# Kernel tuning notes

Measured on AMD Instinct MI355X. Metric: run time of the kernel, lower is better.

Reference implementation:

```python
import jax, jax.numpy as jnp
import numpy as np

CLIP_TEMPERATURE = 1.0


def setup_inputs() -> dict:
    key = jax.random.key(0)
    k1, k2 = jax.random.split(key)
    N, D = 16384, 256
    x = jax.random.normal(k1, (N, D), dtype=jnp.float32)
    y = jax.random.normal(k2, (N, D), dtype=jnp.float32)
    return {"x": x, "y": y}


def reference(x, y):
    # logits[i, j] = <x_i, y_j> / T ; labels are the diagonal (i-th text matches i-th image)
    logits = jnp.einsum('id,jd->ij', x, y) / CLIP_TEMPERATURE  # [N, N]
    N = logits.shape[0]
    diag_idx = jnp.arange(N)
    # CrossEntropy(logits, labels=arange) == -mean(diag(log_softmax(logits, axis=1)))
    lsm_row = jax.nn.log_softmax(logits, axis=1)  # image -> text
    lsm_col = jax.nn.log_softmax(logits, axis=0)  # text  -> image (== log_softmax(logits.T, axis=1).T)
    loss_row = -jnp.mean(lsm_row[diag_idx, diag_idx])
    loss_col = -jnp.mean(lsm_col[diag_idx, diag_idx])
    return (loss_row + loss_col) * 0.5
```

## Files before the change

kernel.cpp:

```cpp
#include <hip/hip_runtime.h>
#include <hip/hip_bf16.h>

#define NN 16384
#define DD 256
#define PANEL 128
#define JCOLS 128
#define BK 32
#define NT 8
#define NJ 16
#define THREADS 256
#define A_BYTES (PANEL * DD * 2)
#define B_BYTES (JCOLS * BK * 2)
#define SHIFT_C 64.0f
#define LOG2E 1.4426950408889634f

typedef __attribute__((ext_vector_type(4))) float f32x4;
typedef __attribute__((ext_vector_type(8))) short bf16x8;

#if __has_builtin(__builtin_amdgcn_exp2f)
#define EXP2F(x) __builtin_amdgcn_exp2f(x)
#else
#define EXP2F(x) exp2f(x)
#endif

__device__ __forceinline__ unsigned pkbf(float a, float b) {
  float2 t; t.x = a; t.y = b;
  __hip_bfloat162 h = __float22bfloat162_rn(t);
  union { __hip_bfloat162 h; unsigned u; } cv;
  cv.h = h;
  return cv.u;
}

__device__ __forceinline__ float rowsum16_dpp(float v) {
  union { float f; int i; } x, t;
  x.f = v;
  t.i = __builtin_amdgcn_update_dpp(0, x.i, 0x111, 0xf, 0xf, true); x.f += t.f;
  t.i = __builtin_amdgcn_update_dpp(0, x.i, 0x112, 0xf, 0xf, true); x.f += t.f;
  t.i = __builtin_amdgcn_update_dpp(0, x.i, 0x114, 0xf, 0xf, true); x.f += t.f;
  t.i = __builtin_amdgcn_update_dpp(0, x.i, 0x118, 0xf, 0xf, true); x.f += t.f;
  return x.f;
}

__global__ __launch_bounds__(256) void cvt_kernel(
    const float* __restrict__ X, const float* __restrict__ Y,
    unsigned short* __restrict__ Xb, unsigned short* __restrict__ Yb) {
  const int groups_per_arr = NN * DD / 8;
  int g = blockIdx.x * 256 + threadIdx.x;
  const float* src;
  unsigned short* dst;
  if (g < groups_per_arr) { src = X; dst = Xb; }
  else { src = Y; dst = Yb; g -= groups_per_arr; }
  float4 a = ((const float4*)src)[(size_t)g * 2];
  float4 b = ((const float4*)src)[(size_t)g * 2 + 1];
  uint4 p = { pkbf(a.x, a.y), pkbf(a.z, a.w), pkbf(b.x, b.y), pkbf(b.z, b.w) };
  ((uint4*)dst)[g] = p;
}

__global__ __launch_bounds__(THREADS, 2) void clip_gemm(
    const unsigned short* __restrict__ Xb, const unsigned short* __restrict__ Yb,
    float* __restrict__ rowsum, float* __restrict__ colsum,
    float* __restrict__ diagsum) {
  __shared__ __align__(16) unsigned char sm[A_BYTES + 2 * B_BYTES];

  const int tid = threadIdx.x;
  const int bid = blockIdx.x;
  const int colgroup = bid & 7;
  const int panel = bid >> 3;
  const int rowbase = panel * PANEL;
  const int colbase = colgroup * (NJ * JCOLS);

  const unsigned short* xb = Xb + (size_t)rowbase * DD;
  const unsigned short* ybg = Yb + (size_t)colbase * DD;

  const int wid = tid >> 6, lane = tid & 63;
  const int wm = wid >> 1, wn = wid & 1;
  const int lm = lane & 15, lk = lane >> 4;

#pragma unroll
  for (int p = 0; p < 16; ++p) {
    const int s = p * 256 + tid;
    const int row = s >> 5;
    const int g = (s & 31) ^ (row & 7);
    __builtin_amdgcn_global_load_lds(
        (const __attribute__((address_space(1))) unsigned*)(xb + row * DD + g * 8),
        (__attribute__((address_space(3))) unsigned*)(sm + s * 16), 16, 0, 0);
  }

  int bsrc[2], bdst[2];
#pragma unroll
  for (int p = 0; p < 2; ++p) {
    const int s = p * 256 + tid;
    const int col = s >> 2;
    const int g = (s & 3) ^ (col & 3);
    bsrc[p] = col * DD + g * 8;
    bdst[p] = A_BYTES + s * 16;
  }

#define GLOADB(jn, tn, buf)                                                    \
  {                                                                            \
    _Pragma("unroll")                                                          \
    for (int p = 0; p < 2; ++p)                                                \
      __builtin_amdgcn_global_load_lds(                                        \
          (const __attribute__((address_space(1))) unsigned*)(ybg + (size_t)(jn) * (JCOLS * DD) + bsrc[p] + (tn) * BK), \
          (__attribute__((address_space(3))) unsigned*)(sm + (buf) * B_BYTES + bdst[p]), \
          16, 0, 0);                                                           \
  }

#define RDA(m, t)                                                              \
  (*(const bf16x8*)(sm + (wm * 64 + (m) * 16 + lm) * (DD * 2) +                \
                    ((((t) * 4 + lk) ^ (lm & 7)) << 4)))
#define RDB(nf, buf)                                                           \
  (*(const bf16x8*)(sm + A_BYTES + (buf) * B_BYTES +                           \
                    (wn * 64 + (nf) * 16 + lm) * (BK * 2) +                    \
                    ((lk ^ (lm & 3)) << 4)))

  f32x4 acc[4][4] = {};
  float rowacc[4][4];
#pragma unroll
  for (int m = 0; m < 4; ++m)
#pragma unroll
    for (int r = 0; r < 4; ++r) rowacc[m][r] = 0.f;
  float dsum = 0.f;
  const float negC = -(SHIFT_C * LOG2E);

  GLOADB(0, 0, 0);

  for (int j = 0; j < NJ; ++j) {
#pragma unroll
    for (int t = 0; t < NT; ++t) {
      __syncthreads();
      if (t < NT - 1) { GLOADB(j, t + 1, (t + 1) & 1); }
      else if (j < NJ - 1) { GLOADB(j + 1, 0, 0); }
      const int buf = t & 1;
      bf16x8 b0[4];
#pragma unroll
      for (int nf = 0; nf < 4; ++nf) b0[nf] = RDB(nf, buf);
#pragma unroll
      for (int m = 0; m < 4; ++m) {
        const bf16x8 a0 = RDA(m, t);
#pragma unroll
        for (int nf = 0; nf < 4; ++nf)
          acc[m][nf] = __builtin_amdgcn_mfma_f32_16x16x32_bf16(a0, b0[nf], acc[m][nf], 0, 0, 0);
      }
    }

    const int jc0 = colbase + j * JCOLS;
    float colacc[4] = {0.f, 0.f, 0.f, 0.f};
#pragma unroll
    for (int m = 0; m < 4; ++m)
#pragma unroll
      for (int nf = 0; nf < 4; ++nf)
#pragma unroll
        for (int r = 0; r < 4; ++r) {
          float e = EXP2F(__builtin_fmaf(acc[m][nf][r], LOG2E, negC));
          rowacc[m][r] += e;
          colacc[nf] += e;
        }
    if (jc0 == rowbase) {
#pragma unroll
      for (int m = 0; m < 4; ++m)
#pragma unroll
        for (int nf = 0; nf < 4; ++nf)
#pragma unroll
          for (int r = 0; r < 4; ++r) {
            const int rr = wm * 64 + m * 16 + lk * 4 + r;
            const int cc = wn * 64 + nf * 16 + lm;
            if (rr == cc) dsum += acc[m][nf][r];
          }
    }
#pragma unroll
    for (int nf = 0; nf < 4; ++nf) {
      float v = colacc[nf];
      v += __shfl_xor(v, 16);
      v += __shfl_xor(v, 32);
      if (lk == 0)
        atomicAdd(&colsum[jc0 + wn * 64 + nf * 16 + lm], v);
    }
    const f32x4 z4 = {0.f, 0.f, 0.f, 0.f};
#pragma unroll
    for (int m = 0; m < 4; ++m)
#pragma unroll
      for (int nf = 0; nf < 4; ++nf) acc[m][nf] = z4;
  }
#undef GLOADB
#undef RDA
#undef RDB

  {
    float d = dsum;
    d += __shfl_xor(d, 1);
    d += __shfl_xor(d, 2);
    d += __shfl_xor(d, 4);
    d += __shfl_xor(d, 8);
    d += __shfl_xor(d, 16);
    d += __shfl_xor(d, 32);
    if (lane == 0 && d != 0.f) atomicAdd(diagsum, d);
  }
#pragma unroll
  for (int m = 0; m < 4; ++m)
#pragma unroll
    for (int r = 0; r < 4; ++r) {
      float v = rowsum16_dpp(rowacc[m][r]);
      if (lm == 15)
        atomicAdd(&rowsum[rowbase + wm * 64 + m * 16 + lk * 4 + r], v);
    }
}

__global__ __launch_bounds__(256) void clip_main_fb(
    const float* __restrict__ X, const float* __restrict__ Y,
    float* __restrict__ rowsum, float* __restrict__ colsum,
    float* __restrict__ diagsum) {
  __shared__ __align__(16) unsigned char smem[2 * 128 * 64 * 2];
  unsigned char* smA = smem;
  unsigned char* smB = smem + 128 * 64 * 2;

  const int tid = threadIdx.x;
  const int bid = blockIdx.x;
  const int swz = (bid & 7) * 2048 + (bid >> 3);
  const int brow = swz >> 7;
  const int bcol = swz & 127;

  const float* xb = X + (size_t)brow * 128 * DD;
  const float* yb = Y + (size_t)bcol * 128 * DD;

  const int wid = tid >> 6, lane = tid & 63;
  const int wm = wid >> 1, wn = wid & 1;
  const int lm = lane & 15, lk = lane >> 4;

  f32x4 acc[4][4] = {};

  for (int ks = 0; ks < 4; ++ks) {
    const int kbase = ks * 64;
    if (ks) __syncthreads();
#pragma unroll
    for (int i = 0; i < 4; ++i) {
      const int c = tid + i * 256;
      const int row = c >> 3, slot = c & 7;
      const int boff = row * 128 + ((slot << 4) ^ ((row & 7) << 4));
      const float* ga = xb + row * DD + kbase + (slot << 3);
      float4 a0 = *(const float4*)ga;
      float4 a1 = *(const float4*)(ga + 4);
      uint4 pa = { pkbf(a0.x, a0.y), pkbf(a0.z, a0.w),
                   pkbf(a1.x, a1.y), pkbf(a1.z, a1.w) };
      *(uint4*)(smA + boff) = pa;
      const float* gb = yb + row * DD + kbase + (slot << 3);
      float4 b0 = *(const float4*)gb;
      float4 b1 = *(const float4*)(gb + 4);
      uint4 pb = { pkbf(b0.x, b0.y), pkbf(b0.z, b0.w),
                   pkbf(b1.x, b1.y), pkbf(b1.z, b1.w) };
      *(uint4*)(smB + boff) = pb;
    }
    __syncthreads();

#pragma unroll
    for (int kk = 0; kk < 2; ++kk) {
      const int kboff = kk * 64 + lk * 16;
      bf16x8 a[4], b[4];
#pragma unroll
      for (int m = 0; m < 4; ++m) {
        const int row = wm * 64 + m * 16 + lm;
        a[m] = *(const bf16x8*)(smA + row * 128 + (kboff ^ ((row & 7) << 4)));
      }
#pragma unroll
      for (int n = 0; n < 4; ++n) {
        const int row = wn * 64 + n * 16 + lm;
        b[n] = *(const bf16x8*)(smB + row * 128 + (kboff ^ ((row & 7) << 4)));
      }
#pragma unroll
      for (int m = 0; m < 4; ++m)
#pragma unroll
        for (int n = 0; n < 4; ++n)
          acc[m][n] = __builtin_amdgcn_mfma_f32_16x16x32_bf16(a[m], b[n], acc[m][n], 0, 0, 0);
    }
  }

  float rowacc[4][4];
  float colacc[4];
#pragma unroll
  for (int m = 0; m < 4; ++m)
#pragma unroll
    for (int r = 0; r < 4; ++r) rowacc[m][r] = 0.f;
#pragma unroll
  for (int n = 0; n < 4; ++n) colacc[n] = 0.f;

  const float negC = -(SHIFT_C * LOG2E);
#pragma unroll
  for (int m = 0; m < 4; ++m)
#pragma unroll
    for (int n = 0; n < 4; ++n)
#pragma unroll
      for (int r = 0; r < 4; ++r) {
        float e = EXP2F(__builtin_fmaf(acc[m][n][r], LOG2E, negC));
        rowacc[m][r] += e;
        colacc[n] += e;
      }

  if (brow == bcol && wm == wn) {
    float dsum = 0.f;
#pragma unroll
    for (int m = 0; m < 4; ++m)
#pragma unroll
      for (int n = 0; n < 4; ++n)
#pragma unroll
        for (int r = 0; r < 4; ++r) {
          const int rr = m * 16 + lk * 4 + r;
          const int cc = n * 16 + lm;
          if (rr == cc) dsum += acc[m][n][r];
        }
    dsum += __shfl_xor(dsum, 1);
    dsum += __shfl_xor(dsum, 2);
    dsum += __shfl_xor(dsum, 4);
    dsum += __shfl_xor(dsum, 8);
    dsum += __shfl_xor(dsum, 16);
    dsum += __shfl_xor(dsum, 32);
    if (lane == 0) atomicAdd(diagsum, dsum);
  }

#pragma unroll
  for (int m = 0; m < 4; ++m)
#pragma unroll
    for (int r = 0; r < 4; ++r) {
      float v = rowsum16_dpp(rowacc[m][r]);
      if (lm == 15)
        atomicAdd(&rowsum[brow * 128 + wm * 64 + m * 16 + lk * 4 + r], v);
    }
#pragma unroll
  for (int n = 0; n < 4; ++n) {
    float v = colacc[n];
    v += __shfl_xor(v, 16);
    v += __shfl_xor(v, 32);
    if (lk == 0)
      atomicAdd(&colsum[bcol * 128 + wn * 64 + n * 16 + lm], v);
  }
}

__global__ __launch_bounds__(256) void clip_stats(
    const float* __restrict__ rowsum, const float* __restrict__ colsum,
    float* __restrict__ partial) {
  __shared__ float sdata[4];
  const int i = blockIdx.x * 256 + threadIdx.x;
  float s = logf(rowsum[i]) + logf(colsum[i]);
  s += __shfl_xor(s, 1);
  s += __shfl_xor(s, 2);
  s += __shfl_xor(s, 4);
  s += __shfl_xor(s, 8);
  s += __shfl_xor(s, 16);
  s += __shfl_xor(s, 32);
  const int lane = threadIdx.x & 63, wv = threadIdx.x >> 6;
  if (lane == 0) sdata[wv] = s;
  __syncthreads();
  if (threadIdx.x == 0)
    atomicAdd(partial, sdata[0] + sdata[1] + sdata[2] + sdata[3]);
}

__global__ void clip_out(const float* __restrict__ partial,
                         const float* __restrict__ diagsum,
                         float* __restrict__ out) {
  if (threadIdx.x == 0)
    out[0] = (float)((double)SHIFT_C + (double)partial[0] * 0.5 / (double)NN
                     - (double)diagsum[0] / (double)NN);
}

extern "C" void kernel_launch(void* const* d_in, const int* in_sizes, int n_in,
                              void* d_out, int out_size, void* d_ws, size_t ws_size,
                              hipStream_t stream) {
  const float* X = (const float*)d_in[0];
  const float* Y = (const float*)d_in[1];

  const size_t bf16_bytes = (size_t)2 * NN * DD * sizeof(unsigned short);
  const size_t stats_bytes = (size_t)(2 * NN + 2) * sizeof(float);

  if (ws_size >= bf16_bytes + stats_bytes) {
    unsigned short* Xb = (unsigned short*)d_ws;
    unsigned short* Yb = Xb + (size_t)NN * DD;
    float* rowsum = (float*)((unsigned char*)d_ws + bf16_bytes);
    float* colsum = rowsum + NN;
    float* diagsum = colsum + NN;
    float* partial = diagsum + 1;

    hipMemsetAsync(rowsum, 0, stats_bytes, stream);
    cvt_kernel<<<dim3(2 * NN * DD / 8 / 256), dim3(256), 0, stream>>>(X, Y, Xb, Yb);
    clip_gemm<<<dim3((NN / PANEL) * 8), dim3(THREADS), 0, stream>>>(
        Xb, Yb, rowsum, colsum, diagsum);
    clip_stats<<<dim3(NN / 256), dim3(256), 0, stream>>>(rowsum, colsum, partial);
    clip_out<<<dim3(1), dim3(64), 0, stream>>>(partial, diagsum, (float*)d_out);
  } else {
    float* rowsum = (float*)d_ws;
    float* colsum = rowsum + NN;
    float* diagsum = colsum + NN;
    float* partial = diagsum + 1;
    hipMemsetAsync(d_ws, 0, stats_bytes, stream);
    clip_main_fb<<<dim3((NN / 128) * (NN / 128)), dim3(256), 0, stream>>>(
        X, Y, rowsum, colsum, diagsum);
    clip_stats<<<dim3(NN / 256), dim3(256), 0, stream>>>(rowsum, colsum, partial);
    clip_out<<<dim3(1), dim3(64), 0, stream>>>(partial, diagsum, (float*)d_out);
  }
}
```

Before: 194.1 us.

## Software-pipeline LDS fragment reads one k-step ahead of MFMA compute

Restructures the inner loop so the A/B fragments for step t are read from LDS into a two-slot register buffer while the MFMAs for step t-1 run. The exp/colsum epilogue for each column tile is deferred into the first step of the next tile. This is meant to hide LDS read latency behind matrix-core work and overlap the epilogue with the next tile's loads. It raises register pressure, since two fragment sets are live, and makes the barrier and buffer ordering more intricate.

Result: no change. 193.7 us (-0.2%).

```diff
diff --git a/kernel.cpp b/kernel.cpp
--- a/kernel.cpp
+++ b/kernel.cpp
@@ -114,6 +114,57 @@
                     (wn * 64 + (nf) * 16 + lm) * (BK * 2) +                    \
                     ((lk ^ (lm & 3)) << 4)))
 
+#define MFMA_STEP(par)                                                         \
+  {                                                                            \
+    _Pragma("unroll")                                                          \
+    for (int m = 0; m < 4; ++m)                                                \
+      _Pragma("unroll")                                                        \
+      for (int nf = 0; nf < 4; ++nf)                                           \
+        acc[m][nf] = __builtin_amdgcn_mfma_f32_16x16x32_bf16(                  \
+            aP[par][m], bP[par][nf], acc[m][nf], 0, 0, 0);                     \
+  }
+
+#define EPILOGUE(jp)                                                           \
+  {                                                                            \
+    const int jc0 = colbase + (jp) * JCOLS;                                    \
+    float colacc[4] = {0.f, 0.f, 0.f, 0.f};                                    \
+    _Pragma("unroll")                                                          \
+    for (int m = 0; m < 4; ++m)                                                \
+      _Pragma("unroll")                                                        \
+      for (int nf = 0; nf < 4; ++nf)                                           \
+        _Pragma("unroll")                                                      \
+        for (int r = 0; r < 4; ++r) {                                          \
+          float e = EXP2F(__builtin_fmaf(acc[m][nf][r], LOG2E, negC));         \
+          rowacc[m][r] += e;                                                   \
+          colacc[nf] += e;                                                     \
+        }                                                                      \
+    if (jc0 == rowbase) {                                                      \
+      _Pragma("unroll")                                                        \
+      for (int m = 0; m < 4; ++m)                                              \
+        _Pragma("unroll")                                                      \
+        for (int nf = 0; nf < 4; ++nf)                                         \
+          _Pragma("unroll")                                                    \
+          for (int r = 0; r < 4; ++r) {                                        \
+            const int rr = wm * 64 + m * 16 + lk * 4 + r;                      \
+            const int cc = wn * 64 + nf * 16 + lm;                             \
+            if (rr == cc) dsum += acc[m][nf][r];                               \
+          }                                                                    \
+    }                                                                          \
+    _Pragma("unroll")                                                          \
+    for (int nf = 0; nf < 4; ++nf) {                                           \
+      float v = colacc[nf];                                                    \
+      v += __shfl_xor(v, 16);                                                  \
+      v += __shfl_xor(v, 32);                                                  \
+      if (lk == 0)                                                             \
+        atomicAdd(&colsum[jc0 + wn * 64 + nf * 16 + lm], v);                   \
+    }                                                                          \
+    const f32x4 z4 = {0.f, 0.f, 0.f, 0.f};                                     \
+    _Pragma("unroll")                                                          \
+    for (int m = 0; m < 4; ++m)                                                \
+      _Pragma("unroll")                                                        \
+      for (int nf = 0; nf < 4; ++nf) acc[m][nf] = z4;                          \
+  }
+
   f32x4 acc[4][4] = {};
   float rowacc[4][4];
 #pragma unroll
@@ -123,68 +174,37 @@
   float dsum = 0.f;
   const float negC = -(SHIFT_C * LOG2E);
 
+  bf16x8 aP[2][4], bP[2][4];
+
   GLOADB(0, 0, 0);
+  __syncthreads();
 
   for (int j = 0; j < NJ; ++j) {
 #pragma unroll
     for (int t = 0; t < NT; ++t) {
-      __syncthreads();
+      if (t > 0) { __syncthreads(); }
+      else if (j > 0) { __syncthreads(); }
       if (t < NT - 1) { GLOADB(j, t + 1, (t + 1) & 1); }
       else if (j < NJ - 1) { GLOADB(j + 1, 0, 0); }
-      const int buf = t & 1;
-      bf16x8 b0[4];
-#pragma unroll
-      for (int nf = 0; nf < 4; ++nf) b0[nf] = RDB(nf, buf);
-#pragma unroll
-      for (int m = 0; m < 4; ++m) {
-        const bf16x8 a0 = RDA(m, t);
-#pragma unroll
-        for (int nf = 0; nf < 4; ++nf)
-          acc[m][nf] = __builtin_amdgcn_mfma_f32_16x16x32_bf16(a0, b0[nf], acc[m][nf], 0, 0, 0);
+#pragma unroll
+      for (int nf = 0; nf < 4; ++nf) bP[t & 1][nf] = RDB(nf, t & 1);
+#pragma unroll
+      for (int m = 0; m < 4; ++m) aP[t & 1][m] = RDA(m, t);
+      if (t > 0) {
+        MFMA_STEP((t - 1) & 1);
+      } else if (j > 0) {
+        MFMA_STEP(1);
+        EPILOGUE(j - 1);
       }
     }
-
-    const int jc0 = colbase + j * JCOLS;
-    float colacc[4] = {0.f, 0.f, 0.f, 0.f};
-#pragma unroll
-    for (int m = 0; m < 4; ++m)
-#pragma unroll
-      for (int nf = 0; nf < 4; ++nf)
-#pragma unroll
-        for (int r = 0; r < 4; ++r) {
-          float e = EXP2F(__builtin_fmaf(acc[m][nf][r], LOG2E, negC));
-          rowacc[m][r] += e;
-          colacc[nf] += e;
-        }
-    if (jc0 == rowbase) {
-#pragma unroll
-      for (int m = 0; m < 4; ++m)
-#pragma unroll
-        for (int nf = 0; nf < 4; ++nf)
-#pragma unroll
-          for (int r = 0; r < 4; ++r) {
-            const int rr = wm * 64 + m * 16 + lk * 4 + r;
-            const int cc = wn * 64 + nf * 16 + lm;
-            if (rr == cc) dsum += acc[m][nf][r];
-          }
-    }
-#pragma unroll
-    for (int nf = 0; nf < 4; ++nf) {
-      float v = colacc[nf];
-      v += __shfl_xor(v, 16);
-      v += __shfl_xor(v, 32);
-      if (lk == 0)
-        atomicAdd(&colsum[jc0 + wn * 64 + nf * 16 + lm], v);
-    }
-    const f32x4 z4 = {0.f, 0.f, 0.f, 0.f};
-#pragma unroll
-    for (int m = 0; m < 4; ++m)
-#pragma unroll
-      for (int nf = 0; nf < 4; ++nf) acc[m][nf] = z4;
-  }
+  }
+  MFMA_STEP(1);
+  EPILOGUE(NJ - 1);
 #undef GLOADB
 #undef RDA
 #undef RDB
+#undef MFMA_STEP
+#undef EPILOGUE
 
   {
     float d = dsum;
```
